# Kernel tuning notes

Measured on AMD Instinct MI355X. Metric: run time of the kernel, lower is better.

## Reference

```python
import jax, jax.numpy as jnp
import numpy as np

B = 32768
W = 7            # window_size (fixed: classifier head outputs 7*2 -> view(B, 7, 2))
F = 80           # per-frame feature size
WF = W * F       # window_feature_size = 560
EH = 512         # encoder_hidden_size
EO = 512         # encoder_output_size
H = 512          # core_hidden_size
NUM_STEPS = 7
EPS = 1e-5

def _linear(x, w, b):
    return x @ w.T + b

def _bn(x, g, bt, m, v):
    # BatchNorm1d in eval mode (running stats)
    return (x - m) * g / jnp.sqrt(v + EPS) + bt

def _ln(x, g, b):
    mu = x.mean(-1, keepdims=True)
    var = x.var(-1, keepdims=True)
    return (x - mu) / jnp.sqrt(var + EPS) * g + b

def setup_inputs():
    key = jax.random.key(0)
    ks = iter(jax.random.split(key, 40))
    def rn(shape, s=0.05):
        return jax.random.normal(next(ks), shape, dtype=jnp.float32) * s
    def rv(shape):
        return jax.random.uniform(next(ks), shape, dtype=jnp.float32) + 0.5
    return {
        'features': jax.random.normal(next(ks), (B, W, F), dtype=jnp.float32),
        'dec_w': rn((W, H)), 'dec_b': rn((W,)),
        'dec_bn_g': rv((W,)), 'dec_bn_b': rn((W,)), 'dec_bn_m': rn((W,)), 'dec_bn_v': rv((W,)),
        'ea1_w': rn((EH, W)), 'ea1_b': rn((EH,)),
        'ea1_bn_g': rv((EH,)), 'ea1_bn_b': rn((EH,)), 'ea1_bn_m': rn((EH,)), 'ea1_bn_v': rv((EH,)),
        'ea2_w': rn((EO, EH)), 'ea2_b': rn((EO,)),
        'ea2_bn_g': rv((EO,)), 'ea2_bn_b': rn((EO,)), 'ea2_bn_m': rn((EO,)), 'ea2_bn_v': rv((EO,)),
        'ei1_w': rn((EH, WF)), 'ei1_b': rn((EH,)),
        'ei1_bn_g': rv((EH,)), 'ei1_bn_b': rn((EH,)), 'ei1_bn_m': rn((EH,)), 'ei1_bn_v': rv((EH,)),
        'ei2_w': rn((EO, EH)), 'ei2_b': rn((EO,)),
        'ei2_bn_g': rv((EO,)), 'ei2_bn_b': rn((EO,)), 'ei2_bn_m': rn((EO,)), 'ei2_bn_v': rv((EO,)),
        'w_ih': rn((4 * H, EO)), 'w_hh': rn((4 * H, H)), 'b_ih': rn((4 * H,)), 'b_hh': rn((4 * H,)),
        'ln_g': rv((H,)), 'ln_b': rn((H,)),
        'cls_w': rn((2 * W, H)), 'cls_b': rn((2 * W,)),
    }

def _forward(features, dec_w, dec_b, dec_bn_g, dec_bn_b, dec_bn_m, dec_bn_v,
             ea1_w, ea1_b, ea1_bn_g, ea1_bn_b, ea1_bn_m, ea1_bn_v,
             ea2_w, ea2_b, ea2_bn_g, ea2_bn_b, ea2_bn_m, ea2_bn_v,
             ei1_w, ei1_b, ei1_bn_g, ei1_bn_b, ei1_bn_m, ei1_bn_v,
             ei2_w, ei2_b, ei2_bn_g, ei2_bn_b, ei2_bn_m, ei2_bn_v,
             w_ih, w_hh, b_ih, b_hh, ln_g, ln_b, cls_w, cls_b):
    Bsz = features.shape[0]

    def encoder(att):
        # attention branch: Linear -> BN -> ReLU -> Linear -> BN
        a = jax.nn.relu(_bn(_linear(att, ea1_w, ea1_b), ea1_bn_g, ea1_bn_b, ea1_bn_m, ea1_bn_v))
        a = _bn(_linear(a, ea2_w, ea2_b), ea2_bn_g, ea2_bn_b, ea2_bn_m, ea2_bn_v)
        # attended-input branch on flattened (features * att)
        ai = (features * att[:, :, None]).reshape(Bsz, WF)
        x = jax.nn.relu(_bn(_linear(ai, ei1_w, ei1_b), ei1_bn_g, ei1_bn_b, ei1_bn_m, ei1_bn_v))
        x = _bn(_linear(x, ei2_w, ei2_b), ei2_bn_g, ei2_bn_b, ei2_bn_m, ei2_bn_v)
        return jax.nn.relu(a + x)

    def lstm_step(x, h, c):
        gates = x @ w_ih.T + b_ih + h @ w_hh.T + b_hh  # [B, 4H], torch gate order i,f,g,o
        i, f, g, o = jnp.split(gates, 4, axis=-1)
        c = jax.nn.sigmoid(f) * c + jax.nn.sigmoid(i) * jnp.tanh(g)
        h = jax.nn.sigmoid(o) * jnp.tanh(c)
        return h, c

    # initial pass: uniform attention, zero LSTM state (state=None -> no LN)
    att0 = jnp.full((Bsz, W), 1.0 / W, dtype=features.dtype)
    h, c = lstm_step(encoder(att0), jnp.zeros((Bsz, H), features.dtype), jnp.zeros((Bsz, H), features.dtype))

    def body(carry, _):
        h, c = carry
        # decoder: Linear -> BN -> smooth softmax
        logits = _bn(_linear(h, dec_w, dec_b), dec_bn_g, dec_bn_b, dec_bn_m, dec_bn_v)
        s = jax.nn.sigmoid(logits)
        att = s / s.sum(-1, keepdims=True)
        agg = encoder(att)
        hn, cn = lstm_step(agg, _ln(h, ln_g, ln_b), _ln(c, ln_g, ln_b))
        return (hn, cn), None

    (h, c), _ = jax.lax.scan(body, (h, c), None, length=NUM_STEPS)
    out = _linear(h, cls_w, cls_b).reshape(Bsz, W, 2)
    return jax.nn.log_softmax(out, axis=2)

def reference(features, dec_w, dec_b, dec_bn_g, dec_bn_b, dec_bn_m, dec_bn_v,
              ea1_w, ea1_b, ea1_bn_g, ea1_bn_b, ea1_bn_m, ea1_bn_v,
              ea2_w, ea2_b, ea2_bn_g, ea2_bn_b, ea2_bn_m, ea2_bn_v,
              ei1_w, ei1_b, ei1_bn_g, ei1_bn_b, ei1_bn_m, ei1_bn_v,
              ei2_w, ei2_b, ei2_bn_g, ei2_bn_b, ei2_bn_m, ei2_bn_v,
              w_ih, w_hh, b_ih, b_hh, ln_g, ln_b, cls_w, cls_b):
    return _forward(features, dec_w, dec_b, dec_bn_g, dec_bn_b, dec_bn_m, dec_bn_v,
                    ea1_w, ea1_b, ea1_bn_g, ea1_bn_b, ea1_bn_m, ea1_bn_v,
                    ea2_w, ea2_b, ea2_bn_g, ea2_bn_b, ea2_bn_m, ea2_bn_v,
                    ei1_w, ei1_b, ei1_bn_g, ei1_bn_b, ei1_bn_m, ei1_bn_v,
                    ei2_w, ei2_b, ei2_bn_g, ei2_bn_b, ei2_bn_m, ei2_bn_v,
                    w_ih, w_hh, b_ih, b_hh, ln_g, ln_b, cls_w, cls_b)
```

## Files before the change

kernel.cpp:

```cpp
#include <hip/hip_runtime.h>
#include <cstdint>
#include <cstddef>

#define BSZ 32768
#define WN 7
#define WF 560
#define K1P 576
#define EPS 1e-5f

typedef __attribute__((ext_vector_type(8))) short bf16x8;
typedef __attribute__((ext_vector_type(4))) float f32x4;

__device__ __forceinline__ float b2f(short s) {
  union { float f; unsigned u; } x; x.u = ((unsigned)(unsigned short)s) << 16; return x.f;
}
__device__ __forceinline__ short f2b(float f) {
  union { float f; unsigned u; } x; x.f = f;
  unsigned r = x.u + 0x7fffu + ((x.u >> 16) & 1u);
  return (short)(r >> 16);
}
__device__ __forceinline__ float sigf(float x) { return 1.0f / (1.0f + __expf(-x)); }
__device__ __forceinline__ float ftanh(float x) {
  float t = __expf(-2.0f * fabsf(x));
  float r = (1.0f - t) / (1.0f + t);
  return copysignf(r, x);
}

__device__ __forceinline__ void async_copy16(const short* g, short* l) {
  __builtin_amdgcn_global_load_lds((const __attribute__((address_space(1))) unsigned*)g,
                                   (__attribute__((address_space(3))) unsigned*)l, 16, 0, 0);
}


__global__ void fold_small_k(const float* __restrict__ dec_w, const float* __restrict__ dec_b,
                             const float* __restrict__ dec_g, const float* __restrict__ dec_bt,
                             const float* __restrict__ dec_m, const float* __restrict__ dec_v,
                             const float* __restrict__ ea1_w, const float* __restrict__ ea1_b,
                             const float* __restrict__ ea1_g, const float* __restrict__ ea1_bt,
                             const float* __restrict__ ea1_m, const float* __restrict__ ea1_v,
                             float* __restrict__ decwf, float* __restrict__ decb8,
                             float* __restrict__ ea1f)
{
  int t = blockIdx.x * 256 + threadIdx.x;
  if (t < 7 * 512) {
    int w = t >> 9;
    float s = dec_g[w] * rsqrtf(dec_v[w] + EPS);
    decwf[t] = dec_w[t] * s;
  }
  if (t < 8) {
    if (t < 7) {
      float s = dec_g[t] * rsqrtf(dec_v[t] + EPS);
      decb8[t] = (dec_b[t] - dec_m[t]) * s + dec_bt[t];
    } else decb8[t] = 0.0f;
  }
  if (t < 512) {
    float s = ea1_g[t] * rsqrtf(ea1_v[t] + EPS);
    #pragma unroll
    for (int w = 0; w < 7; ++w) ea1f[t * 8 + w] = ea1_w[t * 7 + w] * s;
    ea1f[t * 8 + 7] = (ea1_b[t] - ea1_m[t]) * s + ea1_bt[t];
  }
}

__global__ void fold_ei1_k(const float* __restrict__ w, const float* __restrict__ b,
                           const float* __restrict__ g, const float* __restrict__ bt,
                           const float* __restrict__ m, const float* __restrict__ v,
                           short* __restrict__ ei1f, float* __restrict__ bias1)
{
  int idx = blockIdx.x * 256 + threadIdx.x;
  int n = idx / K1P, k = idx % K1P;
  float s = g[n] * rsqrtf(v[n] + EPS);
  ei1f[idx] = (k < WF) ? f2b(w[n * WF + k] * s) : (short)0;
  if (k == 0) bias1[n] = (b[n] - m[n]) * s + bt[n];
}

__global__ void fold_w2_k(const float* __restrict__ wi, const float* __restrict__ bi,
                          const float* __restrict__ gi, const float* __restrict__ bti,
                          const float* __restrict__ mi, const float* __restrict__ vi,
                          const float* __restrict__ wa, const float* __restrict__ ba,
                          const float* __restrict__ ga, const float* __restrict__ bta,
                          const float* __restrict__ ma, const float* __restrict__ va,
                          short* __restrict__ W2, float* __restrict__ bias2)
{
  int idx = blockIdx.x * 256 + threadIdx.x;
  int n = idx >> 10, k = idx & 1023;
  float si = gi[n] * rsqrtf(vi[n] + EPS);
  float sa = ga[n] * rsqrtf(va[n] + EPS);
  float val = (k < 512) ? wi[n * 512 + k] * si : wa[n * 512 + (k - 512)] * sa;
  W2[idx] = f2b(val);
  if (k == 0)
    bias2[n] = (bi[n] - mi[n]) * si + bti[n] + (ba[n] - ma[n]) * sa + bta[n];
}

__global__ void fold_wg_k(const float* __restrict__ w_ih, const float* __restrict__ w_hh,
                          const float* __restrict__ b_ih, const float* __restrict__ b_hh,
                          short* __restrict__ Wg, float* __restrict__ biasg)
{
  int idx = blockIdx.x * 256 + threadIdx.x;
  int c = idx >> 10, k = idx & 1023;
  int g = (c >> 4) & 3;
  int u = (c >> 6) * 16 + (c & 15);
  int r = g * 512 + u;
  float val = (k < 512) ? w_ih[r * 512 + k] : w_hh[r * 512 + (k - 512)];
  Wg[idx] = f2b(val);
  if (k == 0) biasg[c] = b_ih[r] + b_hh[r];
}

__global__ __launch_bounds__(512)
void attln_k(const float* __restrict__ hbuf, const float* __restrict__ cbuf,
             const float* __restrict__ decwf, const float* __restrict__ decb8,
             const float* __restrict__ ea1f,
             const float* __restrict__ ln_g, const float* __restrict__ ln_b,
             const float* __restrict__ feat,
             short* __restrict__ ghA, short* __restrict__ c_ln,
             short* __restrict__ xa, short* __restrict__ ai, int init)
{
  const int lane = threadIdx.x & 63;
  const int b = blockIdx.x * 8 + (threadIdx.x >> 6);
  float av[WN];
  if (init) {
    const float c7 = 1.0f / 7.0f;
    #pragma unroll
    for (int w = 0; w < WN; ++w) av[w] = c7;
    int4 z = make_int4(0, 0, 0, 0);
    *(int4*)&ghA[b * 1024 + 512 + lane * 8] = z;
    *(int4*)&c_ln[b * 512 + lane * 8] = z;
  } else {
    float hl[8];
    const float* hp = hbuf + (size_t)b * 512 + lane * 8;
    *(float4*)&hl[0] = *(const float4*)hp;
    *(float4*)&hl[4] = *(const float4*)(hp + 4);
    float s = 0.f, s2 = 0.f;
    #pragma unroll
    for (int e = 0; e < 8; ++e) { s += hl[e]; s2 += hl[e] * hl[e]; }
    float p[WN];
    #pragma unroll
    for (int w = 0; w < WN; ++w) {
      const float* dw = decwf + w * 512 + lane * 8;
      float4 w0 = *(const float4*)dw, w1 = *(const float4*)(dw + 4);
      p[w] = hl[0] * w0.x + hl[1] * w0.y + hl[2] * w0.z + hl[3] * w0.w
           + hl[4] * w1.x + hl[5] * w1.y + hl[6] * w1.z + hl[7] * w1.w;
    }
    #pragma unroll
    for (int o = 32; o > 0; o >>= 1) {
      s  += __shfl_xor(s, o);
      s2 += __shfl_xor(s2, o);
      #pragma unroll
      for (int w = 0; w < WN; ++w) p[w] += __shfl_xor(p[w], o);
    }
    float mu = s * (1.0f / 512.0f);
    float var = s2 * (1.0f / 512.0f) - mu * mu;
    float rstd = rsqrtf(var + EPS);
    float ssum = 0.f;
    #pragma unroll
    for (int w = 0; w < WN; ++w) { float sg = sigf(p[w] + decb8[w]); av[w] = sg; ssum += sg; }
    float inv = 1.0f / ssum;
    #pragma unroll
    for (int w = 0; w < WN; ++w) av[w] *= inv;
    short o8[8];
    #pragma unroll
    for (int e = 0; e < 8; ++e) {
      int i = lane * 8 + e;
      o8[e] = f2b((hl[e] - mu) * rstd * ln_g[i] + ln_b[i]);
    }
    *(int4*)&ghA[b * 1024 + 512 + lane * 8] = *(int4*)o8;
    float cl[8];
    const float* cp = cbuf + (size_t)b * 512 + lane * 8;
    *(float4*)&cl[0] = *(const float4*)cp;
    *(float4*)&cl[4] = *(const float4*)(cp + 4);
    float cs = 0.f, cs2 = 0.f;
    #pragma unroll
    for (int e = 0; e < 8; ++e) { cs += cl[e]; cs2 += cl[e] * cl[e]; }
    #pragma unroll
    for (int o = 32; o > 0; o >>= 1) {
      cs  += __shfl_xor(cs, o);
      cs2 += __shfl_xor(cs2, o);
    }
    float cmu = cs * (1.0f / 512.0f);
    float cvar = cs2 * (1.0f / 512.0f) - cmu * cmu;
    float crstd = rsqrtf(cvar + EPS);
    #pragma unroll
    for (int e = 0; e < 8; ++e) {
      int i = lane * 8 + e;
      o8[e] = f2b((cl[e] - cmu) * crstd * ln_g[i] + ln_b[i]);
    }
    *(int4*)&c_ln[b * 512 + lane * 8] = *(int4*)o8;
  }
  short a8[8];
  #pragma unroll
  for (int e = 0; e < 8; ++e) {
    int n = lane * 8 + e;
    const float* wr = ea1f + n * 8;
    float4 w0 = *(const float4*)wr, w1 = *(const float4*)(wr + 4);
    float v = w1.w
            + av[0] * w0.x + av[1] * w0.y + av[2] * w0.z + av[3] * w0.w
            + av[4] * w1.x + av[5] * w1.y + av[6] * w1.z;
    a8[e] = f2b(fmaxf(v, 0.0f));
  }
  *(int4*)&xa[b * 1024 + 512 + lane * 8] = *(int4*)a8;
  const float* fr = feat + (size_t)b * WF;
  short* air = ai + (size_t)b * K1P;
  #pragma unroll
  for (int rr = 0; rr < 2; ++rr) {
    int c8 = lane + rr * 64;
    if (c8 < 72) {
      int k = c8 * 8;
      short s8[8];
      if (k < WF) {
        int window = c8 / 10;
        float a = av[0];
        #pragma unroll
        for (int w = 1; w < WN; ++w) a = (window == w) ? av[w] : a;
        float4 f0 = *(const float4*)(fr + k);
        float4 f1 = *(const float4*)(fr + k + 4);
        s8[0] = f2b(f0.x * a); s8[1] = f2b(f0.y * a); s8[2] = f2b(f0.z * a); s8[3] = f2b(f0.w * a);
        s8[4] = f2b(f1.x * a); s8[5] = f2b(f1.y * a); s8[6] = f2b(f1.z * a); s8[7] = f2b(f1.w * a);
      } else {
        #pragma unroll
        for (int e = 0; e < 8; ++e) s8[e] = 0;
      }
      *(int4*)&air[k] = *(int4*)s8;
    }
  }
}


#define E_STAGE(g) do {                                                              \
    short* dA_ = &sA[((g) & 1) * 8192];                                              \
    short* dB_ = &sB[((g) & 1) * 8192];                                              \
    _Pragma("unroll")                                                                \
    for (int q_ = 0; q_ < 4; ++q_) {                                                 \
      int idx_ = q_ * 256 + t;                                                       \
      int row_ = idx_ >> 3, dcol_ = (idx_ & 7) * 8;                                  \
      int scol_ = dcol_ ^ ((row_ & 7) << 3);                                         \
      async_copy16(Ab + (size_t)row_ * lda + (g) * 64 + scol_, dA_ + idx_ * 8);      \
    }                                                                                \
    _Pragma("unroll")                                                                \
    for (int q_ = 0; q_ < 4; ++q_) {                                                 \
      int idx_ = q_ * 256 + t;                                                       \
      int row_ = idx_ >> 3, dcol_ = (idx_ & 7) * 8;                                  \
      int scol_ = dcol_ ^ ((row_ & 7) << 3);                                         \
      async_copy16(Wb + (size_t)row_ * K + (g) * 64 + scol_, dB_ + idx_ * 8);        \
    }                                                                                \
  } while (0)

#define READ_FRAGB(BASE, ROW, KS) \
  (*(const bf16x8*)&BASE[(ROW) * 64 + (((KS)) ^ (((ROW) & 7) << 3))])

template<int KT>
__global__ __launch_bounds__(256)
void gemm_bt_k(const short* __restrict__ A, int lda,
               const short* __restrict__ Wt, int K,
               const float* __restrict__ bias,
               short* __restrict__ C, int ldc)
{
  const int bswz = blockIdx.x;
  const int xcd = bswz & 7, slot = bswz >> 3;
  const int m0 = (xcd + 8 * (slot >> 2)) * 128;
  const int n0 = (slot & 3) * 128;
  __shared__ short sA[2 * 128 * 64];
  __shared__ short sB[2 * 128 * 64];
  const int t = threadIdx.x;
  const int wv = t >> 6, lane = t & 63;
  const int wm = (wv & 1) * 64, wn = (wv >> 1) * 64;
  const int lr = lane & 15, lk = (lane >> 4) * 8;

  f32x4 acc[4][4] = {};
  const short* Ab = A + (size_t)m0 * lda;
  const short* Wb = Wt + (size_t)n0 * K;

  E_STAGE(0);
  asm volatile("s_waitcnt vmcnt(0)" ::: "memory");
  __builtin_amdgcn_s_barrier();

  #pragma unroll
  for (int g = 0; g < KT; ++g) {
    const short* bA_ = &sA[(g & 1) * 8192];
    const short* bB_ = &sB[(g & 1) * 8192];
    if (g + 1 < KT) E_STAGE(g + 1);
    #pragma unroll
    for (int ks = 0; ks < 64; ks += 32) {
      bf16x8 af[4], bfr[4];
      #pragma unroll
      for (int i = 0; i < 4; ++i) af[i]  = READ_FRAGB(bA_, wm + i * 16 + lr, ks + lk);
      #pragma unroll
      for (int j = 0; j < 4; ++j) bfr[j] = READ_FRAGB(bB_, wn + j * 16 + lr, ks + lk);
      #pragma unroll
      for (int i = 0; i < 4; ++i)
        #pragma unroll
        for (int j = 0; j < 4; ++j)
          acc[i][j] = __builtin_amdgcn_mfma_f32_16x16x32_bf16(af[i], bfr[j], acc[i][j], 0, 0, 0);
    }
    if (g + 1 < KT) {
      asm volatile("s_waitcnt vmcnt(0)" ::: "memory");
      __builtin_amdgcn_s_barrier();
    }
  }
  #pragma unroll
  for (int j = 0; j < 4; ++j) {
    int col = n0 + wn + j * 16 + lr;
    float bs = bias[col];
    #pragma unroll
    for (int i = 0; i < 4; ++i) {
      int rbase = m0 + wm + i * 16 + (lane >> 4) * 4;
      #pragma unroll
      for (int e = 0; e < 4; ++e) {
        float v = acc[i][j][e] + bs;
        C[(size_t)(rbase + e) * ldc + col] = f2b(fmaxf(v, 0.0f));
      }
    }
  }
}


#define GS_STAGE(g) do {                                                             \
    short* dA_ = &sA[((g) & 1) * 16384];                                             \
    short* dB_ = &sB[((g) & 1) * 16384];                                             \
    _Pragma("unroll")                                                                \
    for (int q_ = 0; q_ < 4; ++q_) {                                                 \
      int idx_ = q_ * 512 + t;                                                       \
      int row_ = idx_ >> 3, ds_ = idx_ & 7;                                          \
      int sc_ = (ds_ ^ (row_ & 7)) * 8;                                              \
      async_copy16(A + (size_t)(m0 + row_) * 1024 + (g) * 64 + sc_, dA_ + idx_ * 8); \
    }                                                                                \
    _Pragma("unroll")                                                                \
    for (int q_ = 0; q_ < 4; ++q_) {                                                 \
      int idx_ = q_ * 512 + t;                                                       \
      int row_ = idx_ >> 3, ds_ = idx_ & 7;                                          \
      int sc_ = (ds_ ^ (row_ & 7)) * 8;                                              \
      async_copy16(Wg + (size_t)(n0 + row_) * 1024 + (g) * 64 + sc_, dB_ + idx_ * 8);\
    }                                                                                \
  } while (0)

#define GS_COMPUTE(g) do {                                                           \
    const short* bA_ = &sA[((g) & 1) * 16384];                                       \
    const short* bB_ = &sB[((g) & 1) * 16384];                                       \
    _Pragma("unroll")                                                                \
    for (int ks_ = 0; ks_ < 2; ++ks_) {                                              \
      bf16x8 af_[4], bf_[8];                                                         \
      _Pragma("unroll")                                                              \
      for (int mf_ = 0; mf_ < 4; ++mf_) {                                            \
        int row_ = wm * 64 + mf_ * 16 + lr;                                          \
        af_[mf_] = *(const bf16x8*)&bA_[row_ * 64 + (((ks_ * 4 + hi) ^ (row_ & 7)) * 8)]; \
      }                                                                              \
      _Pragma("unroll")                                                              \
      for (int nf_ = 0; nf_ < 8; ++nf_) {                                            \
        int row_ = wn * 128 + nf_ * 16 + lr;                                         \
        bf_[nf_] = *(const bf16x8*)&bB_[row_ * 64 + (((ks_ * 4 + hi) ^ (row_ & 7)) * 8)]; \
      }                                                                              \
      __builtin_amdgcn_s_setprio(1);                                                 \
      _Pragma("unroll")                                                              \
      for (int mf_ = 0; mf_ < 4; ++mf_)                                              \
        _Pragma("unroll")                                                            \
        for (int nf_ = 0; nf_ < 8; ++nf_)                                            \
          acc[mf_][nf_] = __builtin_amdgcn_mfma_f32_16x16x32_bf16(af_[mf_], bf_[nf_], acc[mf_][nf_], 0, 0, 0); \
      __builtin_amdgcn_s_setprio(0);                                                 \
    }                                                                                \
  } while (0)

__global__ __launch_bounds__(512, 2)
void gates_k(const short* __restrict__ A,
             const short* __restrict__ Wg,
             const float* __restrict__ biasg,
             const short* __restrict__ c_ln,
             float* __restrict__ hbuf, float* __restrict__ cbuf)
{
  __shared__ short sA[2 * 256 * 64];
  __shared__ short sB[2 * 256 * 64];
  const int m0 = blockIdx.x * 256;
  const int n0 = blockIdx.y * 256;
  const int t = threadIdx.x;
  const int wid = t >> 6, lane = t & 63;
  const int wm = wid >> 1, wn = wid & 1;
  const int lr = lane & 15, hi = lane >> 4;

  f32x4 acc[4][8] = {};

  GS_STAGE(0);
  asm volatile("s_waitcnt vmcnt(0)" ::: "memory");
  __builtin_amdgcn_s_barrier();

  #pragma unroll
  for (int g = 0; g < 16; ++g) {
    if (g + 1 < 16) GS_STAGE(g + 1);
    GS_COMPUTE(g);
    if (g + 1 < 16) {
      asm volatile("s_waitcnt vmcnt(0) lgkmcnt(0)" ::: "memory");
      __builtin_amdgcn_s_barrier();
    }
  }

  #pragma unroll
  for (int grp = 0; grp < 2; ++grp) {
    const int cb = n0 + wn * 128 + grp * 64;
    const int u = ((cb >> 6)) * 16 + lr;
    const float bi_ = biasg[cb + 0 * 16 + lr];
    const float bf2 = biasg[cb + 1 * 16 + lr];
    const float bg_ = biasg[cb + 2 * 16 + lr];
    const float bo_ = biasg[cb + 3 * 16 + lr];
    #pragma unroll
    for (int mf = 0; mf < 4; ++mf) {
      int rbase = m0 + wm * 64 + mf * 16 + hi * 4;
      #pragma unroll
      for (int e = 0; e < 4; ++e) {
        int row = rbase + e;
        float iv = sigf(acc[mf][grp * 4 + 0][e] + bi_);
        float fv = sigf(acc[mf][grp * 4 + 1][e] + bf2);
        float gv = ftanh(acc[mf][grp * 4 + 2][e] + bg_);
        float ov = sigf(acc[mf][grp * 4 + 3][e] + bo_);
        float cold = b2f(c_ln[(size_t)row * 512 + u]);
        float cc = fv * cold + iv * gv;
        hbuf[(size_t)row * 512 + u] = ov * ftanh(cc);
        cbuf[(size_t)row * 512 + u] = cc;
      }
    }
  }
}

__global__ __launch_bounds__(512)
void cls_k(const float* __restrict__ hbuf, const float* __restrict__ cw,
           const float* __restrict__ cb, float* __restrict__ out)
{
  const int lane = threadIdx.x & 63;
  const int b = blockIdx.x * 8 + (threadIdx.x >> 6);
  float hl[8];
  const float* hp = hbuf + (size_t)b * 512 + lane * 8;
  *(float4*)&hl[0] = *(const float4*)hp;
  *(float4*)&hl[4] = *(const float4*)(hp + 4);
  float p[14];
  #pragma unroll
  for (int tcol = 0; tcol < 14; ++tcol) {
    const float* wr = cw + tcol * 512 + lane * 8;
    float4 w0 = *(const float4*)wr, w1 = *(const float4*)(wr + 4);
    p[tcol] = hl[0] * w0.x + hl[1] * w0.y + hl[2] * w0.z + hl[3] * w0.w
            + hl[4] * w1.x + hl[5] * w1.y + hl[6] * w1.z + hl[7] * w1.w;
  }
  #pragma unroll
  for (int o = 32; o > 0; o >>= 1)
    #pragma unroll
    for (int tcol = 0; tcol < 14; ++tcol) p[tcol] += __shfl_xor(p[tcol], o);
  if (lane < 14) {
    float z = cb[lane];
    #pragma unroll
    for (int tcol = 0; tcol < 14; ++tcol) if (lane == tcol) z += p[tcol];
    float zp = __shfl_xor(z, 1);
    float m = fmaxf(z, zp);
    float l = m + __logf(__expf(z - m) + __expf(zp - m));
    out[(size_t)b * 14 + lane] = z - l;
  }
}


extern "C" void kernel_launch(void* const* d_in, const int* in_sizes, int n_in,
                              void* d_out, int out_size, void* d_ws, size_t ws_size,
                              hipStream_t stream)
{
  const float* features = (const float*)d_in[0];
  const float* dec_w    = (const float*)d_in[1];
  const float* dec_b    = (const float*)d_in[2];
  const float* dec_bn_g = (const float*)d_in[3];
  const float* dec_bn_b = (const float*)d_in[4];
  const float* dec_bn_m = (const float*)d_in[5];
  const float* dec_bn_v = (const float*)d_in[6];
  const float* ea1_w    = (const float*)d_in[7];
  const float* ea1_b    = (const float*)d_in[8];
  const float* ea1_bn_g = (const float*)d_in[9];
  const float* ea1_bn_b = (const float*)d_in[10];
  const float* ea1_bn_m = (const float*)d_in[11];
  const float* ea1_bn_v = (const float*)d_in[12];
  const float* ea2_w    = (const float*)d_in[13];
  const float* ea2_b    = (const float*)d_in[14];
  const float* ea2_bn_g = (const float*)d_in[15];
  const float* ea2_bn_b = (const float*)d_in[16];
  const float* ea2_bn_m = (const float*)d_in[17];
  const float* ea2_bn_v = (const float*)d_in[18];
  const float* ei1_w    = (const float*)d_in[19];
  const float* ei1_b    = (const float*)d_in[20];
  const float* ei1_bn_g = (const float*)d_in[21];
  const float* ei1_bn_b = (const float*)d_in[22];
  const float* ei1_bn_m = (const float*)d_in[23];
  const float* ei1_bn_v = (const float*)d_in[24];
  const float* ei2_w    = (const float*)d_in[25];
  const float* ei2_b    = (const float*)d_in[26];
  const float* ei2_bn_g = (const float*)d_in[27];
  const float* ei2_bn_b = (const float*)d_in[28];
  const float* ei2_bn_m = (const float*)d_in[29];
  const float* ei2_bn_v = (const float*)d_in[30];
  const float* w_ih     = (const float*)d_in[31];
  const float* w_hh     = (const float*)d_in[32];
  const float* b_ih     = (const float*)d_in[33];
  const float* b_hh     = (const float*)d_in[34];
  const float* ln_g     = (const float*)d_in[35];
  const float* ln_b     = (const float*)d_in[36];
  const float* cls_w    = (const float*)d_in[37];
  const float* cls_b    = (const float*)d_in[38];
  (void)in_sizes; (void)n_in; (void)out_size;

  int chunk = BSZ;
  while (chunk > 2048 && (size_t)chunk * 10368 + (16u << 20) > ws_size) chunk >>= 1;

  char* ws = (char*)d_ws;
  size_t off = 0;
  auto carve = [&](size_t bytes) -> void* {
    void* p = ws + off;
    off += (bytes + 255) & ~(size_t)255;
    return p;
  };
  short* ei1f  = (short*)carve((size_t)512 * K1P * 2);
  float* bias1 = (float*)carve(512 * 4);
  short* W2    = (short*)carve((size_t)512 * 1024 * 2);
  float* bias2 = (float*)carve(512 * 4);
  short* Wg    = (short*)carve((size_t)2048 * 1024 * 2);
  float* biasg = (float*)carve(2048 * 4);
  float* decwf = (float*)carve(7 * 512 * 4);
  float* decb8 = (float*)carve(8 * 4);
  float* ea1f  = (float*)carve(512 * 8 * 4);
  float* hbuf  = (float*)carve((size_t)chunk * 512 * 4);
  float* cbuf  = (float*)carve((size_t)chunk * 512 * 4);
  short* ghA   = (short*)carve((size_t)chunk * 1024 * 2);
  short* xa    = (short*)carve((size_t)chunk * 1024 * 2);
  short* clnb  = (short*)carve((size_t)chunk * 512 * 2);
  short* ai    = (short*)carve((size_t)chunk * K1P * 2);

  fold_small_k<<<16, 256, 0, stream>>>(dec_w, dec_b, dec_bn_g, dec_bn_b, dec_bn_m, dec_bn_v,
                                       ea1_w, ea1_b, ea1_bn_g, ea1_bn_b, ea1_bn_m, ea1_bn_v,
                                       decwf, decb8, ea1f);
  fold_ei1_k<<<(512 * K1P) / 256, 256, 0, stream>>>(ei1_w, ei1_b, ei1_bn_g, ei1_bn_b,
                                                    ei1_bn_m, ei1_bn_v, ei1f, bias1);
  fold_w2_k<<<(512 * 1024) / 256, 256, 0, stream>>>(ei2_w, ei2_b, ei2_bn_g, ei2_bn_b, ei2_bn_m, ei2_bn_v,
                                                    ea2_w, ea2_b, ea2_bn_g, ea2_bn_b, ea2_bn_m, ea2_bn_v,
                                                    W2, bias2);
  fold_wg_k<<<(2048 * 1024) / 256, 256, 0, stream>>>(w_ih, w_hh, b_ih, b_hh, Wg, biasg);

  for (int base = 0; base < BSZ; base += chunk) {
    const float* featc = features + (size_t)base * WF;
    float* outc = (float*)d_out + (size_t)base * 14;
    for (int s = 0; s < 8; ++s) {
      attln_k<<<chunk / 8, 512, 0, stream>>>(hbuf, cbuf, decwf, decb8, ea1f, ln_g, ln_b,
                                             featc, ghA, clnb, xa, ai, (s == 0) ? 1 : 0);
      gemm_bt_k<9><<<(chunk / 128) * 4, 256, 0, stream>>>(ai, K1P, ei1f, K1P, bias1, xa, 1024);
      gemm_bt_k<16><<<(chunk / 128) * 4, 256, 0, stream>>>(xa, 1024, W2, 1024, bias2, ghA, 1024);
      gates_k<<<dim3(chunk / 256, 8), 512, 0, stream>>>(ghA, Wg, biasg, clnb, hbuf, cbuf);
    }
    cls_k<<<chunk / 8, 512, 0, stream>>>(hbuf, cls_w, cls_b, outc);
  }
}
```

Before: 2.689 ms.

## Fuse attention scaling of features into first encoder GEMM; store h as bf16

```diff
diff --git a/kernel.cpp b/kernel.cpp
--- a/kernel.cpp
+++ b/kernel.cpp
@@ -106,13 +106,12 @@
 }
 
 __global__ __launch_bounds__(512)
-void attln_k(const float* __restrict__ hbuf, const float* __restrict__ cbuf,
+void attln_k(const short* __restrict__ hb, const float* __restrict__ cbuf,
              const float* __restrict__ decwf, const float* __restrict__ decb8,
              const float* __restrict__ ea1f,
              const float* __restrict__ ln_g, const float* __restrict__ ln_b,
-             const float* __restrict__ feat,
              short* __restrict__ ghA, short* __restrict__ c_ln,
-             short* __restrict__ xa, short* __restrict__ ai, int init)
+             short* __restrict__ xa, float* __restrict__ attb, int init)
 {
   const int lane = threadIdx.x & 63;
   const int b = blockIdx.x * 8 + (threadIdx.x >> 6);
@@ -126,9 +125,10 @@
     *(int4*)&c_ln[b * 512 + lane * 8] = z;
   } else {
     float hl[8];
-    const float* hp = hbuf + (size_t)b * 512 + lane * 8;
-    *(float4*)&hl[0] = *(const float4*)hp;
-    *(float4*)&hl[4] = *(const float4*)(hp + 4);
+    int4 hv = *(const int4*)&hb[(size_t)b * 512 + lane * 8];
+    const short* hs = (const short*)&hv;
+    #pragma unroll
+    for (int e = 0; e < 8; ++e) hl[e] = b2f(hs[e]);
     float s = 0.f, s2 = 0.f;
     #pragma unroll
     for (int e = 0; e < 8; ++e) { s += hl[e]; s2 += hl[e] * hl[e]; }
@@ -184,6 +184,12 @@
       o8[e] = f2b((cl[e] - cmu) * crstd * ln_g[i] + ln_b[i]);
     }
     *(int4*)&c_ln[b * 512 + lane * 8] = *(int4*)o8;
+  }
+  if (lane < 8) {
+    float v = 0.0f;
+    #pragma unroll
+    for (int w = 0; w < WN; ++w) if (lane == w) v = av[w];
+    attb[b * 8 + lane] = v;
   }
   short a8[8];
   #pragma unroll
@@ -197,61 +203,63 @@
     a8[e] = f2b(fmaxf(v, 0.0f));
   }
   *(int4*)&xa[b * 1024 + 512 + lane * 8] = *(int4*)a8;
-  const float* fr = feat + (size_t)b * WF;
-  short* air = ai + (size_t)b * K1P;
-  #pragma unroll
-  for (int rr = 0; rr < 2; ++rr) {
-    int c8 = lane + rr * 64;
-    if (c8 < 72) {
-      int k = c8 * 8;
-      short s8[8];
-      if (k < WF) {
-        int window = c8 / 10;
-        float a = av[0];
-        #pragma unroll
-        for (int w = 1; w < WN; ++w) a = (window == w) ? av[w] : a;
-        float4 f0 = *(const float4*)(fr + k);
-        float4 f1 = *(const float4*)(fr + k + 4);
-        s8[0] = f2b(f0.x * a); s8[1] = f2b(f0.y * a); s8[2] = f2b(f0.z * a); s8[3] = f2b(f0.w * a);
-        s8[4] = f2b(f1.x * a); s8[5] = f2b(f1.y * a); s8[6] = f2b(f1.z * a); s8[7] = f2b(f1.w * a);
-      } else {
-        #pragma unroll
-        for (int e = 0; e < 8; ++e) s8[e] = 0;
-      }
-      *(int4*)&air[k] = *(int4*)s8;
-    }
-  }
-}
-
-
-#define E_STAGE(g) do {                                                              \
+}
+
+#define READ_FRAGB(BASE, ROW, KS) \
+  (*(const bf16x8*)&BASE[(ROW) * 64 + (((KS)) ^ (((ROW) & 7) << 3))])
+
+
+#define F_LOADA(g) do {                                                              \
+    _Pragma("unroll")                                                                \
+    for (int q_ = 0; q_ < 4; ++q_) {                                                 \
+      int idx_ = q_ * 256 + t;                                                       \
+      int row_ = idx_ >> 3, c8_ = idx_ & 7;                                          \
+      int k_ = (g) * 64 + c8_ * 8;                                                   \
+      if (k_ < WF) {                                                                 \
+        const float* fp_ = feat + (size_t)(m0 + row_) * WF + k_;                     \
+        FR[q_][0] = *(const float4*)fp_;                                             \
+        FR[q_][1] = *(const float4*)(fp_ + 4);                                       \
+        AT[q_] = attb[(m0 + row_) * 8 + (k_ / 80)];                                  \
+      } else {                                                                       \
+        FR[q_][0] = make_float4(0.f, 0.f, 0.f, 0.f);                                 \
+        FR[q_][1] = make_float4(0.f, 0.f, 0.f, 0.f);                                 \
+        AT[q_] = 0.f;                                                                \
+      }                                                                              \
+    }                                                                                \
+  } while (0)
+
+#define F_WRITEA(g) do {                                                             \
     short* dA_ = &sA[((g) & 1) * 8192];                                              \
+    _Pragma("unroll")                                                                \
+    for (int q_ = 0; q_ < 4; ++q_) {                                                 \
+      int idx_ = q_ * 256 + t;                                                       \
+      int row_ = idx_ >> 3, dcol_ = (idx_ & 7) * 8;                                  \
+      int pcol_ = dcol_ ^ ((row_ & 7) << 3);                                         \
+      short s8_[8];                                                                  \
+      float a_ = AT[q_];                                                             \
+      s8_[0] = f2b(FR[q_][0].x * a_); s8_[1] = f2b(FR[q_][0].y * a_);                \
+      s8_[2] = f2b(FR[q_][0].z * a_); s8_[3] = f2b(FR[q_][0].w * a_);                \
+      s8_[4] = f2b(FR[q_][1].x * a_); s8_[5] = f2b(FR[q_][1].y * a_);                \
+      s8_[6] = f2b(FR[q_][1].z * a_); s8_[7] = f2b(FR[q_][1].w * a_);                \
+      *(int4*)&dA_[row_ * 64 + pcol_] = *(int4*)s8_;                                 \
+    }                                                                                \
+  } while (0)
+
+#define F_STAGE_B(g) do {                                                            \
     short* dB_ = &sB[((g) & 1) * 8192];                                              \
     _Pragma("unroll")                                                                \
     for (int q_ = 0; q_ < 4; ++q_) {                                                 \
       int idx_ = q_ * 256 + t;                                                       \
       int row_ = idx_ >> 3, dcol_ = (idx_ & 7) * 8;                                  \
       int scol_ = dcol_ ^ ((row_ & 7) << 3);                                         \
-      async_copy16(Ab + (size_t)row_ * lda + (g) * 64 + scol_, dA_ + idx_ * 8);      \
-    }                                                                                \
-    _Pragma("unroll")                                                                \
-    for (int q_ = 0; q_ < 4; ++q_) {                                                 \
-      int idx_ = q_ * 256 + t;                                                       \
-      int row_ = idx_ >> 3, dcol_ = (idx_ & 7) * 8;                                  \
-      int scol_ = dcol_ ^ ((row_ & 7) << 3);                                         \
-      async_copy16(Wb + (size_t)row_ * K + (g) * 64 + scol_, dB_ + idx_ * 8);        \
+      async_copy16(Wb + (size_t)row_ * K1P + (g) * 64 + scol_, dB_ + idx_ * 8);      \
     }                                                                                \
   } while (0)
 
-#define READ_FRAGB(BASE, ROW, KS) \
-  (*(const bf16x8*)&BASE[(ROW) * 64 + (((KS)) ^ (((ROW) & 7) << 3))])
-
-template<int KT>
 __global__ __launch_bounds__(256)
-void gemm_bt_k(const short* __restrict__ A, int lda,
-               const short* __restrict__ Wt, int K,
-               const float* __restrict__ bias,
-               short* __restrict__ C, int ldc)
+void gemm_feat_k(const float* __restrict__ feat, const float* __restrict__ attb,
+                 const short* __restrict__ ei1f, const float* __restrict__ bias1,
+                 short* __restrict__ xa)
 {
   const int bswz = blockIdx.x;
   const int xcd = bswz & 7, slot = bswz >> 3;
@@ -265,18 +273,20 @@
   const int lr = lane & 15, lk = (lane >> 4) * 8;
 
   f32x4 acc[4][4] = {};
-  const short* Ab = A + (size_t)m0 * lda;
-  const short* Wb = Wt + (size_t)n0 * K;
-
-  E_STAGE(0);
+  const short* Wb = ei1f + (size_t)n0 * K1P;
+  float4 FR[4][2]; float AT[4];
+
+  F_LOADA(0); F_STAGE_B(0);
   asm volatile("s_waitcnt vmcnt(0)" ::: "memory");
+  F_WRITEA(0);
+  asm volatile("s_waitcnt lgkmcnt(0)" ::: "memory");
   __builtin_amdgcn_s_barrier();
 
   #pragma unroll
-  for (int g = 0; g < KT; ++g) {
+  for (int g = 0; g < 9; ++g) {
     const short* bA_ = &sA[(g & 1) * 8192];
     const short* bB_ = &sB[(g & 1) * 8192];
-    if (g + 1 < KT) E_STAGE(g + 1);
+    if (g + 1 < 9) { F_LOADA(g + 1); F_STAGE_B(g + 1); }
     #pragma unroll
     for (int ks = 0; ks < 64; ks += 32) {
       bf16x8 af[4], bfr[4];
@@ -290,7 +300,92 @@
         for (int j = 0; j < 4; ++j)
           acc[i][j] = __builtin_amdgcn_mfma_f32_16x16x32_bf16(af[i], bfr[j], acc[i][j], 0, 0, 0);
     }
-    if (g + 1 < KT) {
+    if (g + 1 < 9) {
+      asm volatile("s_waitcnt vmcnt(0)" ::: "memory");
+      F_WRITEA(g + 1);
+      asm volatile("s_waitcnt lgkmcnt(0)" ::: "memory");
+      __builtin_amdgcn_s_barrier();
+    }
+  }
+  #pragma unroll
+  for (int j = 0; j < 4; ++j) {
+    int col = n0 + wn + j * 16 + lr;
+    float bs = bias1[col];
+    #pragma unroll
+    for (int i = 0; i < 4; ++i) {
+      int rbase = m0 + wm + i * 16 + (lane >> 4) * 4;
+      #pragma unroll
+      for (int e = 0; e < 4; ++e) {
+        float v = acc[i][j][e] + bs;
+        xa[(size_t)(rbase + e) * 1024 + col] = f2b(fmaxf(v, 0.0f));
+      }
+    }
+  }
+}
+
+#define E_STAGE(g) do {                                                              \
+    short* dA_ = &sA[((g) & 1) * 8192];                                              \
+    short* dB_ = &sB[((g) & 1) * 8192];                                              \
+    _Pragma("unroll")                                                                \
+    for (int q_ = 0; q_ < 4; ++q_) {                                                 \
+      int idx_ = q_ * 256 + t;                                                       \
+      int row_ = idx_ >> 3, dcol_ = (idx_ & 7) * 8;                                  \
+      int scol_ = dcol_ ^ ((row_ & 7) << 3);                                         \
+      async_copy16(Ab + (size_t)row_ * 1024 + (g) * 64 + scol_, dA_ + idx_ * 8);     \
+    }                                                                                \
+    _Pragma("unroll")                                                                \
+    for (int q_ = 0; q_ < 4; ++q_) {                                                 \
+      int idx_ = q_ * 256 + t;                                                       \
+      int row_ = idx_ >> 3, dcol_ = (idx_ & 7) * 8;                                  \
+      int scol_ = dcol_ ^ ((row_ & 7) << 3);                                         \
+      async_copy16(Wb + (size_t)row_ * 1024 + (g) * 64 + scol_, dB_ + idx_ * 8);     \
+    }                                                                                \
+  } while (0)
+
+__global__ __launch_bounds__(256)
+void gemm_bt_k(const short* __restrict__ A,
+               const short* __restrict__ Wt,
+               const float* __restrict__ bias,
+               short* __restrict__ C)
+{
+  const int bswz = blockIdx.x;
+  const int xcd = bswz & 7, slot = bswz >> 3;
+  const int m0 = (xcd + 8 * (slot >> 2)) * 128;
+  const int n0 = (slot & 3) * 128;
+  __shared__ short sA[2 * 128 * 64];
+  __shared__ short sB[2 * 128 * 64];
+  const int t = threadIdx.x;
+  const int wv = t >> 6, lane = t & 63;
+  const int wm = (wv & 1) * 64, wn = (wv >> 1) * 64;
+  const int lr = lane & 15, lk = (lane >> 4) * 8;
+
+  f32x4 acc[4][4] = {};
+  const short* Ab = A + (size_t)m0 * 1024;
+  const short* Wb = Wt + (size_t)n0 * 1024;
+
+  E_STAGE(0);
+  asm volatile("s_waitcnt vmcnt(0)" ::: "memory");
+  __builtin_amdgcn_s_barrier();
+
+  #pragma unroll
+  for (int g = 0; g < 16; ++g) {
+    const short* bA_ = &sA[(g & 1) * 8192];
+    const short* bB_ = &sB[(g & 1) * 8192];
+    if (g + 1 < 16) E_STAGE(g + 1);
+    #pragma unroll
+    for (int ks = 0; ks < 64; ks += 32) {
+      bf16x8 af[4], bfr[4];
+      #pragma unroll
+      for (int i = 0; i < 4; ++i) af[i]  = READ_FRAGB(bA_, wm + i * 16 + lr, ks + lk);
+      #pragma unroll
+      for (int j = 0; j < 4; ++j) bfr[j] = READ_FRAGB(bB_, wn + j * 16 + lr, ks + lk);
+      #pragma unroll
+      for (int i = 0; i < 4; ++i)
+        #pragma unroll
+        for (int j = 0; j < 4; ++j)
+          acc[i][j] = __builtin_amdgcn_mfma_f32_16x16x32_bf16(af[i], bfr[j], acc[i][j], 0, 0, 0);
+    }
+    if (g + 1 < 16) {
       asm volatile("s_waitcnt vmcnt(0)" ::: "memory");
       __builtin_amdgcn_s_barrier();
     }
@@ -305,12 +400,11 @@
       #pragma unroll
       for (int e = 0; e < 4; ++e) {
         float v = acc[i][j][e] + bs;
-        C[(size_t)(rbase + e) * ldc + col] = f2b(fmaxf(v, 0.0f));
+        C[(size_t)(rbase + e) * 1024 + col] = f2b(fmaxf(v, 0.0f));
       }
     }
   }
 }
-
 
 #define GS_STAGE(g) do {                                                             \
     short* dA_ = &sA[((g) & 1) * 16384];                                             \
@@ -362,7 +456,7 @@
              const short* __restrict__ Wg,
              const float* __restrict__ biasg,
              const short* __restrict__ c_ln,
-             float* __restrict__ hbuf, float* __restrict__ cbuf)
+             short* __restrict__ hb, float* __restrict__ cbuf)
 {
   __shared__ short sA[2 * 256 * 64];
   __shared__ short sB[2 * 256 * 64];
@@ -409,7 +503,7 @@
         float ov = sigf(acc[mf][grp * 4 + 3][e] + bo_);
         float cold = b2f(c_ln[(size_t)row * 512 + u]);
         float cc = fv * cold + iv * gv;
-        hbuf[(size_t)row * 512 + u] = ov * ftanh(cc);
+        hb[(size_t)row * 512 + u] = f2b(ov * ftanh(cc));
         cbuf[(size_t)row * 512 + u] = cc;
       }
     }
@@ -417,15 +511,16 @@
 }
 
 __global__ __launch_bounds__(512)
-void cls_k(const float* __restrict__ hbuf, const float* __restrict__ cw,
+void cls_k(const short* __restrict__ hb, const float* __restrict__ cw,
            const float* __restrict__ cb, float* __restrict__ out)
 {
   const int lane = threadIdx.x & 63;
   const int b = blockIdx.x * 8 + (threadIdx.x >> 6);
   float hl[8];
-  const float* hp = hbuf + (size_t)b * 512 + lane * 8;
-  *(float4*)&hl[0] = *(const float4*)hp;
-  *(float4*)&hl[4] = *(const float4*)(hp + 4);
+  int4 hv = *(const int4*)&hb[(size_t)b * 512 + lane * 8];
+  const short* hs = (const short*)&hv;
+  #pragma unroll
+  for (int e = 0; e < 8; ++e) hl[e] = b2f(hs[e]);
   float p[14];
   #pragma unroll
   for (int tcol = 0; tcol < 14; ++tcol) {
@@ -496,7 +591,7 @@
   (void)in_sizes; (void)n_in; (void)out_size;
 
   int chunk = BSZ;
-  while (chunk > 2048 && (size_t)chunk * 10368 + (16u << 20) > ws_size) chunk >>= 1;
+  while (chunk > 2048 && (size_t)chunk * 8224 + (16u << 20) > ws_size) chunk >>= 1;
 
   char* ws = (char*)d_ws;
   size_t off = 0;
@@ -514,12 +609,12 @@
   float* decwf = (float*)carve(7 * 512 * 4);
   float* decb8 = (float*)carve(8 * 4);
   float* ea1f  = (float*)carve(512 * 8 * 4);
-  float* hbuf  = (float*)carve((size_t)chunk * 512 * 4);
+  short* hb    = (short*)carve((size_t)chunk * 512 * 2);
   float* cbuf  = (float*)carve((size_t)chunk * 512 * 4);
   short* ghA   = (short*)carve((size_t)chunk * 1024 * 2);
   short* xa    = (short*)carve((size_t)chunk * 1024 * 2);
   short* clnb  = (short*)carve((size_t)chunk * 512 * 2);
-  short* ai    = (short*)carve((size_t)chunk * K1P * 2);
+  float* attb  = (float*)carve((size_t)chunk * 8 * 4);
 
   fold_small_k<<<16, 256, 0, stream>>>(dec_w, dec_b, dec_bn_g, dec_bn_b, dec_bn_m, dec_bn_v,
                                        ea1_w, ea1_b, ea1_bn_g, ea1_bn_b, ea1_bn_m, ea1_bn_v,
@@ -535,12 +630,12 @@
     const float* featc = features + (size_t)base * WF;
     float* outc = (float*)d_out + (size_t)base * 14;
     for (int s = 0; s < 8; ++s) {
-      attln_k<<<chunk / 8, 512, 0, stream>>>(hbuf, cbuf, decwf, decb8, ea1f, ln_g, ln_b,
-                                             featc, ghA, clnb, xa, ai, (s == 0) ? 1 : 0);
-      gemm_bt_k<9><<<(chunk / 128) * 4, 256, 0, stream>>>(ai, K1P, ei1f, K1P, bias1, xa, 1024);
-      gemm_bt_k<16><<<(chunk / 128) * 4, 256, 0, stream>>>(xa, 1024, W2, 1024, bias2, ghA, 1024);
-      gates_k<<<dim3(chunk / 256, 8), 512, 0, stream>>>(ghA, Wg, biasg, clnb, hbuf, cbuf);
-    }
-    cls_k<<<chunk / 8, 512, 0, stream>>>(hbuf, cls_w, cls_b, outc);
-  }
-}
+      attln_k<<<chunk / 8, 512, 0, stream>>>(hb, cbuf, decwf, decb8, ea1f, ln_g, ln_b,
+                                             ghA, clnb, xa, attb, (s == 0) ? 1 : 0);
+      gemm_feat_k<<<(chunk / 128) * 4, 256, 0, stream>>>(featc, attb, ei1f, bias1, xa);
+      gemm_bt_k<<<(chunk / 128) * 4, 256, 0, stream>>>(xa, W2, bias2, ghA);
+      gates_k<<<dim3(chunk / 256, 8), 512, 0, stream>>>(ghA, Wg, biasg, clnb, hb, cbuf);
+    }
+    cls_k<<<chunk / 8, 512, 0, stream>>>(hb, cls_w, cls_b, outc);
+  }
+}
```

Result: slower. 3.379 ms (+25.7%).

## Store LSTM hidden state in bf16 and cap batch chunk at 16384

Applied to the files above, without the earlier changes.

```diff
diff --git a/kernel.cpp b/kernel.cpp
--- a/kernel.cpp
+++ b/kernel.cpp
@@ -106,7 +106,7 @@
 }
 
 __global__ __launch_bounds__(512)
-void attln_k(const float* __restrict__ hbuf, const float* __restrict__ cbuf,
+void attln_k(const short* __restrict__ hb, const float* __restrict__ cbuf,
              const float* __restrict__ decwf, const float* __restrict__ decb8,
              const float* __restrict__ ea1f,
              const float* __restrict__ ln_g, const float* __restrict__ ln_b,
@@ -126,9 +126,10 @@
     *(int4*)&c_ln[b * 512 + lane * 8] = z;
   } else {
     float hl[8];
-    const float* hp = hbuf + (size_t)b * 512 + lane * 8;
-    *(float4*)&hl[0] = *(const float4*)hp;
-    *(float4*)&hl[4] = *(const float4*)(hp + 4);
+    int4 hv = *(const int4*)&hb[(size_t)b * 512 + lane * 8];
+    const short* hs = (const short*)&hv;
+    #pragma unroll
+    for (int e = 0; e < 8; ++e) hl[e] = b2f(hs[e]);
     float s = 0.f, s2 = 0.f;
     #pragma unroll
     for (int e = 0; e < 8; ++e) { s += hl[e]; s2 += hl[e] * hl[e]; }
@@ -223,7 +224,6 @@
   }
 }
 
-
 #define E_STAGE(g) do {                                                              \
     short* dA_ = &sA[((g) & 1) * 8192];                                              \
     short* dB_ = &sB[((g) & 1) * 8192];                                              \
@@ -310,7 +310,6 @@
     }
   }
 }
-
 
 #define GS_STAGE(g) do {                                                             \
     short* dA_ = &sA[((g) & 1) * 16384];                                             \
@@ -362,7 +361,7 @@
              const short* __restrict__ Wg,
              const float* __restrict__ biasg,
              const short* __restrict__ c_ln,
-             float* __restrict__ hbuf, float* __restrict__ cbuf)
+             short* __restrict__ hb, float* __restrict__ cbuf)
 {
   __shared__ short sA[2 * 256 * 64];
   __shared__ short sB[2 * 256 * 64];
@@ -409,7 +408,7 @@
         float ov = sigf(acc[mf][grp * 4 + 3][e] + bo_);
         float cold = b2f(c_ln[(size_t)row * 512 + u]);
         float cc = fv * cold + iv * gv;
-        hbuf[(size_t)row * 512 + u] = ov * ftanh(cc);
+        hb[(size_t)row * 512 + u] = f2b(ov * ftanh(cc));
         cbuf[(size_t)row * 512 + u] = cc;
       }
     }
@@ -417,15 +416,16 @@
 }
 
 __global__ __launch_bounds__(512)
-void cls_k(const float* __restrict__ hbuf, const float* __restrict__ cw,
+void cls_k(const short* __restrict__ hb, const float* __restrict__ cw,
            const float* __restrict__ cb, float* __restrict__ out)
 {
   const int lane = threadIdx.x & 63;
   const int b = blockIdx.x * 8 + (threadIdx.x >> 6);
   float hl[8];
-  const float* hp = hbuf + (size_t)b * 512 + lane * 8;
-  *(float4*)&hl[0] = *(const float4*)hp;
-  *(float4*)&hl[4] = *(const float4*)(hp + 4);
+  int4 hv = *(const int4*)&hb[(size_t)b * 512 + lane * 8];
+  const short* hs = (const short*)&hv;
+  #pragma unroll
+  for (int e = 0; e < 8; ++e) hl[e] = b2f(hs[e]);
   float p[14];
   #pragma unroll
   for (int tcol = 0; tcol < 14; ++tcol) {
@@ -495,8 +495,8 @@
   const float* cls_b    = (const float*)d_in[38];
   (void)in_sizes; (void)n_in; (void)out_size;
 
-  int chunk = BSZ;
-  while (chunk > 2048 && (size_t)chunk * 10368 + (16u << 20) > ws_size) chunk >>= 1;
+  int chunk = 16384;
+  while (chunk > 2048 && (size_t)chunk * 9344 + (16u << 20) > ws_size) chunk >>= 1;
 
   char* ws = (char*)d_ws;
   size_t off = 0;
@@ -514,7 +514,7 @@
   float* decwf = (float*)carve(7 * 512 * 4);
   float* decb8 = (float*)carve(8 * 4);
   float* ea1f  = (float*)carve(512 * 8 * 4);
-  float* hbuf  = (float*)carve((size_t)chunk * 512 * 4);
+  short* hb    = (short*)carve((size_t)chunk * 512 * 2);
   float* cbuf  = (float*)carve((size_t)chunk * 512 * 4);
   short* ghA   = (short*)carve((size_t)chunk * 1024 * 2);
   short* xa    = (short*)carve((size_t)chunk * 1024 * 2);
@@ -535,12 +535,12 @@
     const float* featc = features + (size_t)base * WF;
     float* outc = (float*)d_out + (size_t)base * 14;
     for (int s = 0; s < 8; ++s) {
-      attln_k<<<chunk / 8, 512, 0, stream>>>(hbuf, cbuf, decwf, decb8, ea1f, ln_g, ln_b,
+      attln_k<<<chunk / 8, 512, 0, stream>>>(hb, cbuf, decwf, decb8, ea1f, ln_g, ln_b,
                                              featc, ghA, clnb, xa, ai, (s == 0) ? 1 : 0);
       gemm_bt_k<9><<<(chunk / 128) * 4, 256, 0, stream>>>(ai, K1P, ei1f, K1P, bias1, xa, 1024);
       gemm_bt_k<16><<<(chunk / 128) * 4, 256, 0, stream>>>(xa, 1024, W2, 1024, bias2, ghA, 1024);
-      gates_k<<<dim3(chunk / 256, 8), 512, 0, stream>>>(ghA, Wg, biasg, clnb, hbuf, cbuf);
-    }
-    cls_k<<<chunk / 8, 512, 0, stream>>>(hbuf, cls_w, cls_b, outc);
-  }
-}
+      gates_k<<<dim3(chunk / 256, 8), 512, 0, stream>>>(ghA, Wg, biasg, clnb, hb, cbuf);
+    }
+    cls_k<<<chunk / 8, 512, 0, stream>>>(hb, cls_w, cls_b, outc);
+  }
+}
```

After: 2.719 ms. Within noise of the previous version (+1.1%).
